# Optimization experiments

Hardware: AMD Instinct MI355X
Metric: run time of the kernel (lower is better)

Reference implementation:

```python
import jax, jax.numpy as jnp
import numpy as np

B, N, C, H = 4, 2048, 768, 12
D = C // H  # 64
EPS = 1e-12


def setup_inputs() -> dict:
    key = jax.random.key(0)
    ks = jax.random.split(key, 8)
    s = 0.02
    return {
        "x": jax.random.normal(ks[0], (B, N, C), dtype=jnp.float32),
        "Wq": jax.random.normal(ks[1], (C, C), dtype=jnp.float32) * s,
        "bq": jnp.zeros((C,), dtype=jnp.float32),
        "Wkv": jax.random.normal(ks[2], (C, 2 * C), dtype=jnp.float32) * s,
        "bkv": jnp.zeros((2 * C,), dtype=jnp.float32),
        "Wproj": jax.random.normal(ks[3], (C, C), dtype=jnp.float32) * s,
        "bproj": jnp.zeros((C,), dtype=jnp.float32),
        "scale": jnp.full((1, H, 1, 1), D ** -0.5, dtype=jnp.float32),
    }


def _l2norm(t):
    # F.normalize(dim=-1): x / max(||x||_2, eps)
    n = jnp.sqrt(jnp.sum(t * t, axis=-1, keepdims=True))
    return t / jnp.maximum(n, EPS)


def reference(x, Wq, bq, Wkv, bkv, Wproj, bproj, scale):
    b, n, c = x.shape
    q = (x @ Wq + bq).reshape(b, n, H, D).transpose(0, 2, 1, 3)        # [B,H,N,D]
    kv = (x @ Wkv + bkv).reshape(b, n, 2, H, D).transpose(2, 0, 3, 1, 4)
    k, v = kv[0], kv[1]                                                # [B,H,N,D]
    q = _l2norm(q)
    k = _l2norm(k)
    attn = jnp.einsum("bhqd,bhkd->bhqk", q, k) * scale                 # [B,H,N,N]
    attn = jax.nn.softmax(attn, axis=-1)
    out = jnp.einsum("bhqk,bhkd->bhqd", attn, v)                       # [B,H,N,D]
    out = out.transpose(0, 2, 1, 3).reshape(b, n, c)
    return out @ Wproj + bproj
```

## Files before the change

### kernel.cpp

```cpp
#include <hip/hip_runtime.h>
#include <hip/hip_bf16.h>
#include <math.h>


typedef short bf16x8 __attribute__((ext_vector_type(8)));
typedef float f32x4 __attribute__((ext_vector_type(4)));

static __device__ __forceinline__ unsigned short f2bf(float f) {
    unsigned int u = __float_as_uint(f);
    unsigned int r = u + 0x7fff + ((u >> 16) & 1);
    return (unsigned short)(r >> 16);
}
static __device__ __forceinline__ unsigned int pack2(float a, float b) {
    return (unsigned int)f2bf(a) | ((unsigned int)f2bf(b) << 16);
}
static __device__ __forceinline__ unsigned int cvtpk(float a, float b) {
    unsigned int r;
    asm("v_cvt_pk_bf16_f32 %0, %1, %2" : "=v"(r) : "v"(a), "v"(b));
    return r;
}
static __device__ __forceinline__ void gl_lds16(const void* g, void* l) {
    __builtin_amdgcn_global_load_lds(
        (const __attribute__((address_space(1))) unsigned int*)g,
        (__attribute__((address_space(3))) unsigned int*)l, 16, 0, 0);
}

__global__ __launch_bounds__(256) void convx_kernel(
    const float* __restrict__ in, unsigned short* __restrict__ out)
{
    size_t i = ((size_t)blockIdx.x * 256 + threadIdx.x) * 8;
    float4 a = *(const float4*)&in[i];
    float4 b = *(const float4*)&in[i + 4];
    uint4 o = make_uint4(pack2(a.x, a.y), pack2(a.z, a.w), pack2(b.x, b.y), pack2(b.z, b.w));
    *(uint4*)&out[i] = o;
}

__global__ __launch_bounds__(256) void convT_kernel(
    const float* __restrict__ A, int ldA, const float* __restrict__ Bs, int ldB, int split,
    unsigned short* __restrict__ out)
{
    __shared__ char tb[8192];
    const int c0 = blockIdx.x * 64, k0 = blockIdx.y * 64;
    const int t = threadIdx.x;
    const int kl = t >> 2, cq = (t & 3) * 16;
    const float* src; int ld; int cbase;
    if (c0 < split) { src = A;  ld = ldA; cbase = c0; }
    else            { src = Bs; ld = ldB; cbase = c0 - split; }
    #pragma unroll
    for (int jj = 0; jj < 4; ++jj) {
        float4 v = *(const float4*)&src[(size_t)(k0 + kl) * ld + cbase + cq + jj * 4];
        float vv[4] = {v.x, v.y, v.z, v.w};
        #pragma unroll
        for (int je = 0; je < 4; ++je) {
            int c = cq + jj * 4 + je;
            *(unsigned short*)(tb + c * 128 + ((kl * 2) ^ ((c & 7) << 4))) = f2bf(vv[je]);
        }
    }
    __syncthreads();
    const int cl = t >> 2, u2 = (t & 3) * 2;
    uint4 r0 = *(const uint4*)(tb + cl * 128 + ((u2 ^ (cl & 7)) << 4));
    uint4 r1 = *(const uint4*)(tb + cl * 128 + (((u2 + 1) ^ (cl & 7)) << 4));
    size_t ob = (size_t)(c0 + cl) * 768 + k0 + (t & 3) * 16;
    *(uint4*)&out[ob] = r0;
    *(uint4*)&out[ob + 8] = r1;
}

__global__ __launch_bounds__(256) void qkv_gemm_kernel(
    const unsigned short* __restrict__ xb, const unsigned short* __restrict__ WT,
    const float* __restrict__ bq, const float* __restrict__ bkv,
    const float* __restrict__ scale,
    unsigned short* __restrict__ Qb, unsigned short* __restrict__ Kb,
    unsigned short* __restrict__ Vtb)
{
    __shared__ char lds[32768] __attribute__((aligned(16)));

    const int ct = blockIdx.x;
    const int row0 = blockIdx.y * 128;
    const int tid = threadIdx.x;
    const int w = tid >> 6, l = tid & 63;
    const int g = l >> 4, ln = l & 15;
    const int wr = w >> 1, wc = w & 1;
    const int col0 = ct * 128;

    const int srow = (w & 1) * 64 + (l >> 3);
    const int su = ((l & 7) ^ (l >> 3)) * 16;
    const char* s = (w < 2)
        ? (const char*)xb + (size_t)(row0 + srow) * 1536 + su
        : (const char*)WT + (size_t)(col0 + srow) * 1536 + su;
    char* dbase = lds + ((w >= 2) ? 16384 : 0) + (w & 1) * 8192;

    f32x4 acc[4][4];
    #pragma unroll
    for (int m = 0; m < 4; ++m)
        #pragma unroll
        for (int n = 0; n < 4; ++n) acc[m][n] = (f32x4){0.f, 0.f, 0.f, 0.f};

    const int arow = (wr * 64 + ln) * 128;
    const int brow = 16384 + (wc * 64 + ln) * 128;
    const int x0 = ((0 + g) ^ (ln & 7)) * 16;
    const int x1 = ((4 + g) ^ (ln & 7)) * 16;

    for (int ks = 0; ks < 12; ++ks) {
        __syncthreads();
        #pragma unroll
        for (int j = 0; j < 8; ++j)
            gl_lds16(s + (size_t)j * 8 * 1536, dbase + j * 1024);
        s += 128;
        __syncthreads();
        #pragma unroll
        for (int kc = 0; kc < 2; ++kc) {
            const int xo = kc ? x1 : x0;
            bf16x8 af[4], bfr[4];
            #pragma unroll
            for (int m = 0; m < 4; ++m) af[m] = *(const bf16x8*)(lds + arow + m * 2048 + xo);
            #pragma unroll
            for (int n = 0; n < 4; ++n) bfr[n] = *(const bf16x8*)(lds + brow + n * 2048 + xo);
            #pragma unroll
            for (int m = 0; m < 4; ++m)
                #pragma unroll
                for (int n = 0; n < 4; ++n)
                    acc[m][n] = __builtin_amdgcn_mfma_f32_16x16x32_bf16(af[m], bfr[n], acc[m][n], 0, 0, 0);
        }
    }

    const int co = col0 + wc * 64 + ln;
    float bv[4];
    #pragma unroll
    for (int n = 0; n < 4; ++n) {
        int c = co + n * 16;
        bv[n] = (c < 768) ? bq[c] : bkv[c - 768];
    }
    const int region = ct / 6;
    const int h = (ct % 6) * 2 + wc;

    if (region < 2) {
        unsigned short* dst = (region == 0) ? Qb : Kb;
        const float post = (region == 0) ? scale[0] * 1.4426950408889634f : 1.0f;
        #pragma unroll
        for (int m = 0; m < 4; ++m) {
            #pragma unroll
            for (int n = 0; n < 4; ++n)
                #pragma unroll
                for (int r = 0; r < 4; ++r) acc[m][n][r] += bv[n];
            #pragma unroll
            for (int r = 0; r < 4; ++r) {
                float ss = 0.f;
                #pragma unroll
                for (int n = 0; n < 4; ++n) ss += acc[m][n][r] * acc[m][n][r];
                ss += __shfl_xor(ss, 1); ss += __shfl_xor(ss, 2);
                ss += __shfl_xor(ss, 4); ss += __shfl_xor(ss, 8);
                float inv = post / fmaxf(sqrtf(ss), 1e-12f);
                int t = row0 + wr * 64 + m * 16 + g * 4 + r;
                int b = t >> 11, nt = t & 2047;
                size_t base = ((size_t)(b * 12 + h) * 2048 + nt) * 64 + ln;
                #pragma unroll
                for (int n = 0; n < 4; ++n)
                    dst[base + n * 16] = f2bf(acc[m][n][r] * inv);
            }
        }
    } else {
        char* tb = lds + w * 8192;
        __syncthreads();
        #pragma unroll
        for (int m = 0; m < 4; ++m)
            #pragma unroll
            for (int n = 0; n < 4; ++n)
                #pragma unroll
                for (int r = 0; r < 4; ++r) {
                    int d = n * 16 + ln;
                    int tok = m * 16 + g * 4 + r;
                    *(unsigned short*)(tb + d * 128 + ((tok * 2) ^ ((d & 7) << 4))) =
                        f2bf(acc[m][n][r] + bv[n]);
                }
        __syncthreads();
        const int t0 = row0 + wr * 64;
        const int b = t0 >> 11, n0 = t0 & 2047;
        #pragma unroll
        for (int i = 0; i < 8; ++i) {
            int d = i * 8 + (l >> 3);
            uint4 v = *(const uint4*)(tb + d * 128 + (((l & 7) ^ (d & 7)) << 4));
            *(uint4*)&Vtb[((size_t)(b * 12 + h) * 64 + d) * 2048 + n0 + (l & 7) * 8] = v;
        }
    }
}

__global__ __launch_bounds__(512, 6) void attn_kernel(
    const unsigned short* __restrict__ Qg, const unsigned short* __restrict__ Kg,
    const unsigned short* __restrict__ Vtg,
    unsigned short* __restrict__ O)
{
    __shared__ char lds[49152] __attribute__((aligned(16)));

    const int bid = blockIdx.y * 16 + blockIdx.x;
    const int swzb = (bid & 7) * 96 + (bid >> 3);
    const int bh  = swzb >> 4;
    const int q0  = (swzb & 15) * 128;

    const int tid = threadIdx.x;
    const int w   = tid >> 6;
    const int l   = tid & 63;
    const int g   = l >> 4;
    const int ln  = l & 15;

    const int srow = w * 8 + (l >> 3);
    const int su   = ((l & 7) ^ (l >> 3)) * 16;
    const char* kS = (const char*)Kg  + ((size_t)bh * 2048 + srow) * 128 + su;
    const char* vS = (const char*)Vtg + ((size_t)bh * 64   + srow) * 4096 + su;
    char* kD0 = lds + w * 1024;
    char* vD0 = lds + 16384 + w * 1024;

    bf16x8 qf0, qf1;
    {
        const unsigned short* qp = Qg + ((size_t)bh * 2048 + q0 + w * 16 + ln) * 64 + g * 8;
        qf0 = *(const bf16x8*)qp;
        qf1 = *(const bf16x8*)(qp + 32);
    }

    const int swz = (ln & 7) << 4;
    const int a_rd   = ln * 128 + ((g * 16) ^ swz);
    const int a_rd64 = a_rd ^ 64;
    const int pbase = 32768 + w * 2048;
    const int pw0 = pbase + ln * 128 + ((g * 8) ^ swz);
    const int pr0 = pbase + ln * 128 + ((g * 16) ^ swz);
    const int pr1 = pr0 ^ 64;

    f32x4 oacc[4];
    #pragma unroll
    for (int dn = 0; dn < 4; ++dn) oacc[dn] = (f32x4){0.f, 0.f, 0.f, 0.f};
    float rs = 0.f;

    const f32x4 zero4 = (f32x4){0.f, 0.f, 0.f, 0.f};

    auto compute = [&](const int OFF) {
        f32x4 s[4];
        __builtin_amdgcn_s_setprio(1);
        #pragma unroll
        for (int kn = 0; kn < 4; ++kn) {
            bf16x8 kf0 = *(const bf16x8*)(lds + OFF + kn * 2048 + a_rd);
            bf16x8 kf1 = *(const bf16x8*)(lds + OFF + kn * 2048 + a_rd64);
            s[kn] = __builtin_amdgcn_mfma_f32_16x16x32_bf16(kf0, qf0, zero4, 0, 0, 0);
            s[kn] = __builtin_amdgcn_mfma_f32_16x16x32_bf16(kf1, qf1, s[kn], 0, 0, 0);
        }
        __builtin_amdgcn_s_setprio(0);

        #pragma unroll
        for (int kn = 0; kn < 4; ++kn) {
            float e0 = __builtin_amdgcn_exp2f(s[kn][0]);
            float e1 = __builtin_amdgcn_exp2f(s[kn][1]);
            float e2 = __builtin_amdgcn_exp2f(s[kn][2]);
            float e3 = __builtin_amdgcn_exp2f(s[kn][3]);
            rs += (e0 + e1) + (e2 + e3);
            *(uint2*)(lds + (pw0 ^ (kn << 5))) = make_uint2(cvtpk(e0, e1), cvtpk(e2, e3));
        }

        __builtin_amdgcn_s_setprio(1);
        {
            bf16x8 pf = *(const bf16x8*)(lds + pr0);
            #pragma unroll
            for (int dn = 0; dn < 4; ++dn) {
                bf16x8 vf = *(const bf16x8*)(lds + 16384 + OFF + dn * 2048 + a_rd);
                oacc[dn] = __builtin_amdgcn_mfma_f32_16x16x32_bf16(pf, vf, oacc[dn], 0, 0, 0);
            }
        }
        {
            bf16x8 pf = *(const bf16x8*)(lds + pr1);
            #pragma unroll
            for (int dn = 0; dn < 4; ++dn) {
                bf16x8 vf = *(const bf16x8*)(lds + 16384 + OFF + dn * 2048 + a_rd64);
                oacc[dn] = __builtin_amdgcn_mfma_f32_16x16x32_bf16(pf, vf, oacc[dn], 0, 0, 0);
            }
        }
        __builtin_amdgcn_s_setprio(0);
    };

    gl_lds16(kS, kD0); gl_lds16(vS, vD0);
    kS += 8192; vS += 128;
    __syncthreads();

    #pragma unroll 1
    for (int it = 0; it < 16; ++it) {
        gl_lds16(kS, kD0 + 8192); gl_lds16(vS, vD0 + 8192);
        kS += 8192; vS += 128;
        compute(0);
        __syncthreads();
        if (it < 15) {
            gl_lds16(kS, kD0); gl_lds16(vS, vD0);
            kS += 8192; vS += 128;
        }
        compute(8192);
        __syncthreads();
    }

    const int b = bh / 12, h = bh % 12;
    float v = rs;
    v += __shfl_xor(v, 16); v += __shfl_xor(v, 32);
    #pragma unroll
    for (int r = 0; r < 4; ++r) {
        float inv = 1.0f / __shfl(v, g * 4 + r);
        int qrg = q0 + w * 16 + g * 4 + r;
        size_t base = ((size_t)(b * 2048 + qrg)) * 768 + h * 64;
        #pragma unroll
        for (int dn = 0; dn < 4; ++dn)
            O[base + dn * 16 + ln] = f2bf(oacc[dn][r] * inv);
    }
}

__global__ __launch_bounds__(256) void proj_gemm_kernel(
    const unsigned short* __restrict__ Ob, const unsigned short* __restrict__ WT,
    const float* __restrict__ bp, float* __restrict__ out)
{
    __shared__ char lds[32768] __attribute__((aligned(16)));

    const int row0 = blockIdx.y * 128;
    const int col0 = blockIdx.x * 128;
    const int tid = threadIdx.x;
    const int w = tid >> 6, l = tid & 63;
    const int g = l >> 4, ln = l & 15;
    const int wr = w >> 1, wc = w & 1;

    const int srow = (w & 1) * 64 + (l >> 3);
    const int su = ((l & 7) ^ (l >> 3)) * 16;
    const char* s = (w < 2)
        ? (const char*)Ob + (size_t)(row0 + srow) * 1536 + su
        : (const char*)WT + (size_t)(col0 + srow) * 1536 + su;
    char* dbase = lds + ((w >= 2) ? 16384 : 0) + (w & 1) * 8192;

    f32x4 acc[4][4];
    #pragma unroll
    for (int m = 0; m < 4; ++m)
        #pragma unroll
        for (int n = 0; n < 4; ++n) acc[m][n] = (f32x4){0.f, 0.f, 0.f, 0.f};

    const int arow = (wr * 64 + ln) * 128;
    const int brow = 16384 + (wc * 64 + ln) * 128;
    const int x0 = ((0 + g) ^ (ln & 7)) * 16;
    const int x1 = ((4 + g) ^ (ln & 7)) * 16;

    for (int ks = 0; ks < 12; ++ks) {
        __syncthreads();
        #pragma unroll
        for (int j = 0; j < 8; ++j)
            gl_lds16(s + (size_t)j * 8 * 1536, dbase + j * 1024);
        s += 128;
        __syncthreads();
        #pragma unroll
        for (int kc = 0; kc < 2; ++kc) {
            const int xo = kc ? x1 : x0;
            bf16x8 af[4], bfr[4];
            #pragma unroll
            for (int m = 0; m < 4; ++m) af[m] = *(const bf16x8*)(lds + arow + m * 2048 + xo);
            #pragma unroll
            for (int n = 0; n < 4; ++n) bfr[n] = *(const bf16x8*)(lds + brow + n * 2048 + xo);
            #pragma unroll
            for (int m = 0; m < 4; ++m)
                #pragma unroll
                for (int n = 0; n < 4; ++n)
                    acc[m][n] = __builtin_amdgcn_mfma_f32_16x16x32_bf16(af[m], bfr[n], acc[m][n], 0, 0, 0);
        }
    }

    const int co = col0 + wc * 64 + ln;
    float bv[4];
    #pragma unroll
    for (int n = 0; n < 4; ++n) bv[n] = bp[co + n * 16];
    #pragma unroll
    for (int m = 0; m < 4; ++m)
        #pragma unroll
        for (int r = 0; r < 4; ++r) {
            int t = row0 + wr * 64 + m * 16 + g * 4 + r;
            #pragma unroll
            for (int n = 0; n < 4; ++n)
                out[(size_t)t * 768 + co + n * 16] = acc[m][n][r] + bv[n];
        }
}

extern "C" void kernel_launch(void* const* d_in, const int* in_sizes, int n_in,
                              void* d_out, int out_size, void* d_ws, size_t ws_size,
                              hipStream_t stream) {
    const float* x     = (const float*)d_in[0];
    const float* Wq    = (const float*)d_in[1];
    const float* bq    = (const float*)d_in[2];
    const float* Wkv   = (const float*)d_in[3];
    const float* bkv   = (const float*)d_in[4];
    const float* Wp    = (const float*)d_in[5];
    const float* bp    = (const float*)d_in[6];
    const float* scale = (const float*)d_in[7];
    float* out = (float*)d_out;

    unsigned short* ws = (unsigned short*)d_ws;
    const size_t SZ = (size_t)4 * 12 * 2048 * 64;
    unsigned short* xbw   = ws;
    unsigned short* WqkvT = xbw + SZ;
    unsigned short* WprjT = WqkvT + (size_t)2304 * 768;
    unsigned short* Qw    = WprjT + (size_t)768 * 768;
    unsigned short* Kw    = Qw + SZ;
    unsigned short* Vtw   = Kw + SZ;
    unsigned short* Ow    = Vtw + SZ;

    convx_kernel<<<3072, 256, 0, stream>>>(x, xbw);
    convT_kernel<<<dim3(36, 12), 256, 0, stream>>>(Wq, 768, Wkv, 1536, 768, WqkvT);
    convT_kernel<<<dim3(12, 12), 256, 0, stream>>>(Wp, 768, Wp, 768, 768, WprjT);
    qkv_gemm_kernel<<<dim3(18, 64), 256, 0, stream>>>(xbw, WqkvT, bq, bkv, scale, Qw, Kw, Vtw);
    attn_kernel<<<dim3(16, 48), 512, 0, stream>>>(Qw, Kw, Vtw, Ow);
    proj_gemm_kernel<<<dim3(6, 64), 256, 0, stream>>>(Ow, WprjT, bp, out);
}
```

Before: 144.7 us.

## Rewrite attention kernel with 32x32 MFMA tiles and register-resident P

Reworks the attention kernel to use 32x32x16 bf16 MFMAs, with 4 waves each owning 32 query rows instead of 8 waves of 16 rows. The exp'd scores are repacked in registers via v_permlane32_swap so they feed the PV MFMA directly. This removes the LDS round trip for P and the LDS space it needed. Each wave now holds more accumulator registers, so occupancy drops, and each thread issues more global-to-LDS loads per tile.

```diff
diff --git a/kernel.cpp b/kernel.cpp
--- a/kernel.cpp
+++ b/kernel.cpp
@@ -5,6 +5,7 @@
 
 typedef short bf16x8 __attribute__((ext_vector_type(8)));
 typedef float f32x4 __attribute__((ext_vector_type(4)));
+typedef float f32x16 __attribute__((ext_vector_type(16)));
 
 static __device__ __forceinline__ unsigned short f2bf(float f) {
     unsigned int u = __float_as_uint(f);
@@ -184,124 +185,135 @@
     }
 }
 
-__global__ __launch_bounds__(512, 6) void attn_kernel(
+__global__ __launch_bounds__(256, 3) void attn_kernel(
     const unsigned short* __restrict__ Qg, const unsigned short* __restrict__ Kg,
     const unsigned short* __restrict__ Vtg,
     unsigned short* __restrict__ O)
 {
-    __shared__ char lds[49152] __attribute__((aligned(16)));
+    __shared__ char lds[32768] __attribute__((aligned(16)));
 
     const int bid = blockIdx.y * 16 + blockIdx.x;
     const int swzb = (bid & 7) * 96 + (bid >> 3);
-    const int bh  = swzb >> 4;
-    const int q0  = (swzb & 15) * 128;
+    const int bh = swzb >> 4;
+    const int q0 = (swzb & 15) * 128;
 
     const int tid = threadIdx.x;
-    const int w   = tid >> 6;
-    const int l   = tid & 63;
-    const int g   = l >> 4;
-    const int ln  = l & 15;
-
-    const int srow = w * 8 + (l >> 3);
+    const int w  = tid >> 6;
+    const int l  = tid & 63;
+    const int lo = l & 31;
+    const int hi = l >> 5;
+
+    const int srow = w * 16 + (l >> 3);
     const int su   = ((l & 7) ^ (l >> 3)) * 16;
     const char* kS = (const char*)Kg  + ((size_t)bh * 2048 + srow) * 128 + su;
     const char* vS = (const char*)Vtg + ((size_t)bh * 64   + srow) * 4096 + su;
-    char* kD0 = lds + w * 1024;
-    char* vD0 = lds + 16384 + w * 1024;
-
-    bf16x8 qf0, qf1;
+    char* kD = lds + w * 2048;
+    char* vD = lds + 16384 + w * 2048;
+
+    bf16x8 qf[4];
     {
-        const unsigned short* qp = Qg + ((size_t)bh * 2048 + q0 + w * 16 + ln) * 64 + g * 8;
-        qf0 = *(const bf16x8*)qp;
-        qf1 = *(const bf16x8*)(qp + 32);
-    }
-
-    const int swz = (ln & 7) << 4;
-    const int a_rd   = ln * 128 + ((g * 16) ^ swz);
-    const int a_rd64 = a_rd ^ 64;
-    const int pbase = 32768 + w * 2048;
-    const int pw0 = pbase + ln * 128 + ((g * 8) ^ swz);
-    const int pr0 = pbase + ln * 128 + ((g * 16) ^ swz);
-    const int pr1 = pr0 ^ 64;
-
-    f32x4 oacc[4];
-    #pragma unroll
-    for (int dn = 0; dn < 4; ++dn) oacc[dn] = (f32x4){0.f, 0.f, 0.f, 0.f};
+        const unsigned short* qp = Qg + ((size_t)bh * 2048 + q0 + w * 32 + lo) * 64 + hi * 8;
+        qf[0] = *(const bf16x8*)(qp);
+        qf[1] = *(const bf16x8*)(qp + 16);
+        qf[2] = *(const bf16x8*)(qp + 32);
+        qf[3] = *(const bf16x8*)(qp + 48);
+    }
+
+    const int swz = (lo & 7) << 4;
+    const int rowb = lo * 128;
+    int coff[4];
+    #pragma unroll
+    for (int c = 0; c < 4; ++c) coff[c] = (c * 32 + hi * 16) ^ swz;
+
+    f32x16 oacc0, oacc1;
+    #pragma unroll
+    for (int r = 0; r < 16; ++r) { oacc0[r] = 0.f; oacc1[r] = 0.f; }
     float rs = 0.f;
 
-    const f32x4 zero4 = (f32x4){0.f, 0.f, 0.f, 0.f};
+    const f32x16 zero16 = {0.f,0.f,0.f,0.f,0.f,0.f,0.f,0.f,0.f,0.f,0.f,0.f,0.f,0.f,0.f,0.f};
 
     auto compute = [&](const int OFF) {
-        f32x4 s[4];
+        const char* Kb = lds + OFF;
+        const char* Vb = lds + 16384 + OFF;
+
+        f32x16 s0, s1;
         __builtin_amdgcn_s_setprio(1);
-        #pragma unroll
-        for (int kn = 0; kn < 4; ++kn) {
-            bf16x8 kf0 = *(const bf16x8*)(lds + OFF + kn * 2048 + a_rd);
-            bf16x8 kf1 = *(const bf16x8*)(lds + OFF + kn * 2048 + a_rd64);
-            s[kn] = __builtin_amdgcn_mfma_f32_16x16x32_bf16(kf0, qf0, zero4, 0, 0, 0);
-            s[kn] = __builtin_amdgcn_mfma_f32_16x16x32_bf16(kf1, qf1, s[kn], 0, 0, 0);
-        }
+        s0 = __builtin_amdgcn_mfma_f32_32x32x16_bf16(*(const bf16x8*)(Kb + rowb + coff[0]), qf[0], zero16, 0, 0, 0);
+        s0 = __builtin_amdgcn_mfma_f32_32x32x16_bf16(*(const bf16x8*)(Kb + rowb + coff[1]), qf[1], s0, 0, 0, 0);
+        s0 = __builtin_amdgcn_mfma_f32_32x32x16_bf16(*(const bf16x8*)(Kb + rowb + coff[2]), qf[2], s0, 0, 0, 0);
+        s0 = __builtin_amdgcn_mfma_f32_32x32x16_bf16(*(const bf16x8*)(Kb + rowb + coff[3]), qf[3], s0, 0, 0, 0);
+        s1 = __builtin_amdgcn_mfma_f32_32x32x16_bf16(*(const bf16x8*)(Kb + 4096 + rowb + coff[0]), qf[0], zero16, 0, 0, 0);
+        s1 = __builtin_amdgcn_mfma_f32_32x32x16_bf16(*(const bf16x8*)(Kb + 4096 + rowb + coff[1]), qf[1], s1, 0, 0, 0);
+        s1 = __builtin_amdgcn_mfma_f32_32x32x16_bf16(*(const bf16x8*)(Kb + 4096 + rowb + coff[2]), qf[2], s1, 0, 0, 0);
+        s1 = __builtin_amdgcn_mfma_f32_32x32x16_bf16(*(const bf16x8*)(Kb + 4096 + rowb + coff[3]), qf[3], s1, 0, 0, 0);
         __builtin_amdgcn_s_setprio(0);
 
         #pragma unroll
-        for (int kn = 0; kn < 4; ++kn) {
-            float e0 = __builtin_amdgcn_exp2f(s[kn][0]);
-            float e1 = __builtin_amdgcn_exp2f(s[kn][1]);
-            float e2 = __builtin_amdgcn_exp2f(s[kn][2]);
-            float e3 = __builtin_amdgcn_exp2f(s[kn][3]);
-            rs += (e0 + e1) + (e2 + e3);
-            *(uint2*)(lds + (pw0 ^ (kn << 5))) = make_uint2(cvtpk(e0, e1), cvtpk(e2, e3));
-        }
-
-        __builtin_amdgcn_s_setprio(1);
-        {
-            bf16x8 pf = *(const bf16x8*)(lds + pr0);
-            #pragma unroll
-            for (int dn = 0; dn < 4; ++dn) {
-                bf16x8 vf = *(const bf16x8*)(lds + 16384 + OFF + dn * 2048 + a_rd);
-                oacc[dn] = __builtin_amdgcn_mfma_f32_16x16x32_bf16(pf, vf, oacc[dn], 0, 0, 0);
+        for (int r = 0; r < 16; ++r) s0[r] = __builtin_amdgcn_exp2f(s0[r]);
+        #pragma unroll
+        for (int r = 0; r < 16; ++r) s1[r] = __builtin_amdgcn_exp2f(s1[r]);
+        float t0 = 0.f, t1 = 0.f;
+        #pragma unroll
+        for (int r = 0; r < 16; ++r) { t0 += s0[r]; t1 += s1[r]; }
+        rs += t0 + t1;
+
+        #pragma unroll
+        for (int kb = 0; kb < 2; ++kb) {
+            const f32x16 ec = kb ? s1 : s0;
+            #pragma unroll
+            for (int ksb = 0; ksb < 2; ++ksb) {
+                const int ks = kb * 2 + ksb;
+                const int rqA = ksb * 2, rqB = rqA + 1;
+                unsigned int uA0 = cvtpk(ec[rqA * 4 + 0], ec[rqA * 4 + 1]);
+                unsigned int uA1 = cvtpk(ec[rqA * 4 + 2], ec[rqA * 4 + 3]);
+                unsigned int uB0 = cvtpk(ec[rqB * 4 + 0], ec[rqB * 4 + 1]);
+                unsigned int uB1 = cvtpk(ec[rqB * 4 + 2], ec[rqB * 4 + 3]);
+                asm("v_permlane32_swap_b32 %0, %1" : "+v"(uA0), "+v"(uB0));
+                asm("v_permlane32_swap_b32 %0, %1" : "+v"(uA1), "+v"(uB1));
+                unsigned int fw[4] = {uA0, uA1, uB0, uB1};
+                bf16x8 pa;
+                __builtin_memcpy(&pa, fw, 16);
+                __builtin_amdgcn_s_setprio(1);
+                bf16x8 v0 = *(const bf16x8*)(Vb + rowb + coff[ks]);
+                bf16x8 v1 = *(const bf16x8*)(Vb + 4096 + rowb + coff[ks]);
+                oacc0 = __builtin_amdgcn_mfma_f32_32x32x16_bf16(pa, v0, oacc0, 0, 0, 0);
+                oacc1 = __builtin_amdgcn_mfma_f32_32x32x16_bf16(pa, v1, oacc1, 0, 0, 0);
+                __builtin_amdgcn_s_setprio(0);
             }
         }
-        {
-            bf16x8 pf = *(const bf16x8*)(lds + pr1);
-            #pragma unroll
-            for (int dn = 0; dn < 4; ++dn) {
-                bf16x8 vf = *(const bf16x8*)(lds + 16384 + OFF + dn * 2048 + a_rd64);
-                oacc[dn] = __builtin_amdgcn_mfma_f32_16x16x32_bf16(pf, vf, oacc[dn], 0, 0, 0);
-            }
-        }
-        __builtin_amdgcn_s_setprio(0);
     };
 
-    gl_lds16(kS, kD0); gl_lds16(vS, vD0);
+    gl_lds16(kS, kD);          gl_lds16(kS + 1024, kD + 1024);
+    gl_lds16(vS, vD);          gl_lds16(vS + 32768, vD + 1024);
     kS += 8192; vS += 128;
     __syncthreads();
 
     #pragma unroll 1
     for (int it = 0; it < 16; ++it) {
-        gl_lds16(kS, kD0 + 8192); gl_lds16(vS, vD0 + 8192);
+        gl_lds16(kS, kD + 8192);          gl_lds16(kS + 1024, kD + 9216);
+        gl_lds16(vS, vD + 8192);          gl_lds16(vS + 32768, vD + 9216);
         kS += 8192; vS += 128;
         compute(0);
         __syncthreads();
         if (it < 15) {
-            gl_lds16(kS, kD0); gl_lds16(vS, vD0);
+            gl_lds16(kS, kD);          gl_lds16(kS + 1024, kD + 1024);
+            gl_lds16(vS, vD);          gl_lds16(vS + 32768, vD + 1024);
             kS += 8192; vS += 128;
         }
         compute(8192);
         __syncthreads();
     }
 
+    float rsv = rs;
+    rsv += __shfl_xor(rsv, 32);
     const int b = bh / 12, h = bh % 12;
-    float v = rs;
-    v += __shfl_xor(v, 16); v += __shfl_xor(v, 32);
-    #pragma unroll
-    for (int r = 0; r < 4; ++r) {
-        float inv = 1.0f / __shfl(v, g * 4 + r);
-        int qrg = q0 + w * 16 + g * 4 + r;
-        size_t base = ((size_t)(b * 2048 + qrg)) * 768 + h * 64;
-        #pragma unroll
-        for (int dn = 0; dn < 4; ++dn)
-            O[base + dn * 16 + ln] = f2bf(oacc[dn][r] * inv);
+    #pragma unroll
+    for (int r = 0; r < 16; ++r) {
+        const int qr = (r & 3) + 8 * (r >> 2) + 4 * hi;
+        float inv = 1.0f / __shfl(rsv, qr);
+        size_t base = ((size_t)(b * 2048 + q0 + w * 32 + qr)) * 768 + h * 64 + lo;
+        O[base]      = f2bf(oacc0[r] * inv);
+        O[base + 32] = f2bf(oacc1[r] * inv);
     }
 }
 
@@ -401,6 +413,6 @@
     convT_kernel<<<dim3(36, 12), 256, 0, stream>>>(Wq, 768, Wkv, 1536, 768, WqkvT);
     convT_kernel<<<dim3(12, 12), 256, 0, stream>>>(Wp, 768, Wp, 768, 768, WprjT);
     qkv_gemm_kernel<<<dim3(18, 64), 256, 0, stream>>>(xbw, WqkvT, bq, bkv, scale, Qw, Kw, Vtw);
-    attn_kernel<<<dim3(16, 48), 512, 0, stream>>>(Qw, Kw, Vtw, Ow);
+    attn_kernel<<<dim3(16, 48), 256, 0, stream>>>(Qw, Kw, Vtw, Ow);
     proj_gemm_kernel<<<dim3(6, 64), 256, 0, stream>>>(Ow, WprjT, bp, out);
 }
```

Result: no change. 145.1 us (+0.3%).
